# Optimization experiments

Hardware: AMD Instinct MI355X
Metric: run time of the kernel (lower is better)

Reference implementation:

```python
import jax, jax.numpy as jnp
import numpy as np

N_NODES = 50000
N_EDGES = 800000
IN_FEATS = 128
H_FEATS = 128
NUM_CLASSES = 16


def setup_inputs() -> dict:
    key = jax.random.key(0)
    ks = jax.random.split(key, 10)
    in_feat = jax.random.normal(ks[0], (N_NODES, IN_FEATS), dtype=jnp.float32)
    src = jax.random.randint(ks[1], (N_EDGES,), 0, N_NODES, dtype=jnp.int64)
    dst = jax.random.randint(ks[2], (N_EDGES,), 0, N_NODES, dtype=jnp.int64)
    def glorot(k, shape):
        lim = np.sqrt(6.0 / (shape[0] + shape[1]))
        return jax.random.uniform(k, shape, jnp.float32, -lim, lim)
    W_self1 = glorot(ks[3], (IN_FEATS, H_FEATS))
    W_neigh1 = glorot(ks[4], (IN_FEATS, H_FEATS))
    b1 = jnp.zeros((H_FEATS,), jnp.float32)
    W_self2 = glorot(ks[5], (H_FEATS, NUM_CLASSES))
    W_neigh2 = glorot(ks[6], (H_FEATS, NUM_CLASSES))
    b2 = jnp.zeros((NUM_CLASSES,), jnp.float32)
    return {"in_feat": in_feat, "src": src, "dst": dst,
            "W_self1": W_self1, "W_neigh1": W_neigh1, "b1": b1,
            "W_self2": W_self2, "W_neigh2": W_neigh2, "b2": b2}


def _mean_agg(h, src, dst, n_nodes):
    # sum of source features at each destination node, divided by in-degree
    summed = jax.ops.segment_sum(h[src], dst, num_segments=n_nodes)  # [N, d]
    deg = jax.ops.segment_sum(jnp.ones_like(dst, dtype=h.dtype), dst,
                              num_segments=n_nodes)                   # [N]
    return summed / jnp.maximum(deg, 1.0)[:, None]


def _sage_conv(h, src, dst, W_self, W_neigh, b):
    h_neigh = _mean_agg(h, src, dst, h.shape[0])
    return h @ W_self + h_neigh @ W_neigh + b


def reference(in_feat, src, dst, W_self1, W_neigh1, b1, W_self2, W_neigh2, b2):
    h = _sage_conv(in_feat, src, dst, W_self1, W_neigh1, b1)
    h = jax.nn.relu(h)
    h = _sage_conv(h, src, dst, W_self2, W_neigh2, b2)
    return h
```

## Files before the change

kernel.cpp:

```cpp
#include <hip/hip_runtime.h>

#define NF 128
#define BSH 8
#define CHUNK 4096

typedef __attribute__((ext_vector_type(8))) short short8;
typedef __attribute__((ext_vector_type(4))) float floatx4;

__device__ __forceinline__ unsigned short f2bf(float f) {
    unsigned u = __float_as_uint(f);
    u += 0x7fff + ((u >> 16) & 1);
    return (unsigned short)(u >> 16);
}
__device__ __forceinline__ unsigned pk2(float a, float b) {
    return (unsigned)f2bf(a) | ((unsigned)f2bf(b) << 16);
}
__device__ __forceinline__ float bflo(unsigned u) { return __uint_as_float(u << 16); }
__device__ __forceinline__ float bfhi(unsigned u) { return __uint_as_float(u & 0xffff0000u); }

__device__ __forceinline__ unsigned enc8(float f) {
    unsigned b = __float_as_uint(f);
    unsigned s = (b >> 24) & 0x80u;
    b &= 0x7fffffffu;
    unsigned t = b + 0x7FFFFu + ((b >> 20) & 1u);
    unsigned m = (t >= 0x3C800000u) ? (((t - 0x3C000000u) >> 20) & 0x7Fu) : 0u;
    return s | m;
}
__device__ __forceinline__ void dec4(float* acc, unsigned w) {
#pragma unroll
    for (int j = 0; j < 4; ++j) {
        unsigned u = (w >> (8 * j)) & 0xffu;
        acc[j] += __uint_as_float(((u & 0x80u) << 24) | ((u & 0x7fu) << 20));
    }
}


__global__ __launch_bounds__(256) void k_prep(const float* __restrict__ in_feat,
                                              const int* __restrict__ dst,
                                              const float* __restrict__ Ws1,
                                              const float* __restrict__ Wn1,
                                              const float* __restrict__ Ws2,
                                              const float* __restrict__ Wn2,
                                              unsigned short* __restrict__ featbf,
                                              unsigned char* __restrict__ feat8,
                                              unsigned short* __restrict__ W1t,
                                              unsigned short* __restrict__ W2t,
                                              int* __restrict__ cnt2,
                                              int nb_cvt, int nb_w, int E) {
    int b = blockIdx.x, tid = threadIdx.x;
    if (b < nb_cvt) {
        int i = b * 256 + tid;
        const float4* p = (const float4*)in_feat + (size_t)i * 2;
        float4 a = p[0], c = p[1];
        uint4 o;
        o.x = pk2(a.x, a.y); o.y = pk2(a.z, a.w);
        o.z = pk2(c.x, c.y); o.w = pk2(c.z, c.w);
        ((uint4*)featbf)[i] = o;
        uint2 q;
        q.x = enc8(a.x) | (enc8(a.y) << 8) | (enc8(a.z) << 16) | (enc8(a.w) << 24);
        q.y = enc8(c.x) | (enc8(c.y) << 8) | (enc8(c.z) << 16) | (enc8(c.w) << 24);
        ((uint2*)feat8)[i] = q;
    } else if (b < nb_cvt + nb_w) {
        int idx = (b - nb_cvt) * 256 + tid;
        if (idx < 128 * 256) {
            int n = idx >> 8, kk = idx & 255;
            float v = (kk < 128) ? Ws1[(size_t)kk * 128 + n]
                                 : Wn1[(size_t)(kk - 128) * 128 + n];
            W1t[idx] = f2bf(v);
        } else {
            int idx2 = idx - 128 * 256;
            if (idx2 < 32 * 128) {
                int n = idx2 >> 7, k = idx2 & 127;
                float v = (n < 16) ? Ws2[(size_t)k * 16 + n]
                                   : Wn2[(size_t)k * 16 + (n - 16)];
                W2t[idx2] = f2bf(v);
            }
        }
    } else {
        __shared__ int h[256];
        int c = b - nb_cvt - nb_w;
        h[tid] = 0;
        __syncthreads();
        int base = c * CHUNK;
        int n = min(CHUNK, E - base);
        for (int i = tid; i < n; i += 256) atomicAdd(&h[dst[base + i] >> BSH], 1);
        __syncthreads();
        cnt2[c * 256 + tid] = h[tid];
    }
}


__global__ __launch_bounds__(256) void k_cscan(const int* __restrict__ cnt2,
                                               int* __restrict__ goff,
                                               int* __restrict__ basep, int nc) {
    __shared__ int sw[4];
    int tid = threadIdx.x, lane = tid & 63, w = tid >> 6;
    int tot = 0;
    int c = 0;
    for (; c + 7 < nc; c += 8) {
        int v0 = cnt2[(c + 0) * 256 + tid], v1 = cnt2[(c + 1) * 256 + tid];
        int v2 = cnt2[(c + 2) * 256 + tid], v3 = cnt2[(c + 3) * 256 + tid];
        int v4 = cnt2[(c + 4) * 256 + tid], v5 = cnt2[(c + 5) * 256 + tid];
        int v6 = cnt2[(c + 6) * 256 + tid], v7 = cnt2[(c + 7) * 256 + tid];
        tot += ((v0 + v1) + (v2 + v3)) + ((v4 + v5) + (v6 + v7));
    }
    for (; c < nc; ++c) tot += cnt2[c * 256 + tid];

    int inc = tot;
#pragma unroll
    for (int d = 1; d < 64; d <<= 1) {
        int t = __shfl_up(inc, (unsigned)d, 64);
        if (lane >= d) inc += t;
    }
    if (lane == 63) sw[w] = inc;
    __syncthreads();
    int add = 0;
    for (int i = 0; i < w; ++i) add += sw[i];
    int ex = add + inc - tot;
    goff[tid] = ex;
    if (tid == 255) goff[256] = ex + tot;

    int run = ex;
    for (c = 0; c < nc; c += 8) {
        int v[8];
#pragma unroll
        for (int j = 0; j < 8; ++j)
            v[j] = (c + j < nc) ? cnt2[(c + j) * 256 + tid] : 0;
#pragma unroll
        for (int j = 0; j < 8; ++j) {
            if (c + j < nc) basep[(c + j) * 256 + tid] = run;
            run += v[j];
        }
    }
}


__global__ __launch_bounds__(256) void k_part(const int* __restrict__ src,
                                              const int* __restrict__ dst,
                                              const int* __restrict__ basep,
                                              unsigned* __restrict__ ebuf, int E) {
    __shared__ int cur[256];
    int tid = threadIdx.x;
    cur[tid] = basep[blockIdx.x * 256 + tid];
    __syncthreads();
    int base = blockIdx.x * CHUNK;
    int n = min(CHUNK, E - base);
    for (int i = tid; i < n; i += 256) {
        int dd = dst[base + i];
        int p = atomicAdd(&cur[dd >> BSH], 1);
        ebuf[p] = ((unsigned)(dd & 255) << 16) | (unsigned)src[base + i];
    }
}


__global__ __launch_bounds__(256) void k_fine(const unsigned* __restrict__ ebuf,
                                              const int* __restrict__ goff,
                                              int* __restrict__ off,
                                              int* __restrict__ csr, int N) {
    __shared__ int degL[256];
    __shared__ int offL[256];
    __shared__ int sw[4];
    int b = blockIdx.x, tid = threadIdx.x;
    int node0 = b << BSH;
    int e0 = goff[b], e1 = goff[b + 1];
    degL[tid] = 0;
    __syncthreads();
    for (int e = e0 + tid; e < e1; e += 256) atomicAdd(&degL[ebuf[e] >> 16], 1);
    __syncthreads();
    int lane = tid & 63, w = tid >> 6;
    int v = degL[tid], inc = v;
#pragma unroll
    for (int d = 1; d < 64; d <<= 1) {
        int t = __shfl_up(inc, (unsigned)d, 64);
        if (lane >= d) inc += t;
    }
    if (lane == 63) sw[w] = inc;
    __syncthreads();
    int add = 0;
    for (int i = 0; i < w; ++i) add += sw[i];
    int ex = add + inc - v;
    offL[tid] = ex;
    int idx = node0 + tid;
    if (idx <= N) off[idx] = e0 + ex;
    degL[tid] = 0;
    __syncthreads();
    for (int e = e0 + tid; e < e1; e += 256) {
        unsigned u = ebuf[e];
        int d = u >> 16;
        int pos = e0 + offL[d] + atomicAdd(&degL[d], 1);
        csr[pos] = (int)(u & 0xffffu);
    }
}


__global__ __launch_bounds__(256, 6) void k_agg1(const unsigned char* __restrict__ feat8,
                                                 const int* __restrict__ off,
                                                 const int* __restrict__ csr,
                                                 unsigned short* __restrict__ hn1,
                                                 int N, int pb) {
    int b = blockIdx.x;
    int half = (b >= pb) ? 1 : 0;
    int idx = (b - half * pb) * 256 + threadIdx.x;
    int g = idx >> 3;
    int lane = idx & 7;
    if (g >= N) return;
    int s0 = off[g], s1 = off[g + 1];
    const unsigned char* base = feat8 + half * 64 + lane * 8;
    float acc[8];
#pragma unroll
    for (int i = 0; i < 8; ++i) acc[i] = 0.f;
    int e = s0;
    for (; e + 7 < s1; e += 8) {
        uint2 v0 = *(const uint2*)(base + (size_t)csr[e + 0] * 128);
        uint2 v1 = *(const uint2*)(base + (size_t)csr[e + 1] * 128);
        uint2 v2 = *(const uint2*)(base + (size_t)csr[e + 2] * 128);
        uint2 v3 = *(const uint2*)(base + (size_t)csr[e + 3] * 128);
        uint2 v4 = *(const uint2*)(base + (size_t)csr[e + 4] * 128);
        uint2 v5 = *(const uint2*)(base + (size_t)csr[e + 5] * 128);
        uint2 v6 = *(const uint2*)(base + (size_t)csr[e + 6] * 128);
        uint2 v7 = *(const uint2*)(base + (size_t)csr[e + 7] * 128);
        dec4(acc + 0, v0.x); dec4(acc + 4, v0.y);
        dec4(acc + 0, v1.x); dec4(acc + 4, v1.y);
        dec4(acc + 0, v2.x); dec4(acc + 4, v2.y);
        dec4(acc + 0, v3.x); dec4(acc + 4, v3.y);
        dec4(acc + 0, v4.x); dec4(acc + 4, v4.y);
        dec4(acc + 0, v5.x); dec4(acc + 4, v5.y);
        dec4(acc + 0, v6.x); dec4(acc + 4, v6.y);
        dec4(acc + 0, v7.x); dec4(acc + 4, v7.y);
    }
    if (e + 3 < s1) {
        uint2 v0 = *(const uint2*)(base + (size_t)csr[e + 0] * 128);
        uint2 v1 = *(const uint2*)(base + (size_t)csr[e + 1] * 128);
        uint2 v2 = *(const uint2*)(base + (size_t)csr[e + 2] * 128);
        uint2 v3 = *(const uint2*)(base + (size_t)csr[e + 3] * 128);
        dec4(acc + 0, v0.x); dec4(acc + 4, v0.y);
        dec4(acc + 0, v1.x); dec4(acc + 4, v1.y);
        dec4(acc + 0, v2.x); dec4(acc + 4, v2.y);
        dec4(acc + 0, v3.x); dec4(acc + 4, v3.y);
        e += 4;
    }
    for (; e < s1; ++e) {
        uint2 v = *(const uint2*)(base + (size_t)csr[e] * 128);
        dec4(acc + 0, v.x); dec4(acc + 4, v.y);
    }
    float inv = __uint_as_float(0x7B800000u) / fmaxf((float)(s1 - s0), 1.0f);
    uint4 o;
    o.x = pk2(acc[0] * inv, acc[1] * inv);
    o.y = pk2(acc[2] * inv, acc[3] * inv);
    o.z = pk2(acc[4] * inv, acc[5] * inv);
    o.w = pk2(acc[6] * inv, acc[7] * inv);
    *(uint4*)(hn1 + (size_t)g * NF + half * 64 + lane * 8) = o;
}


__global__ __launch_bounds__(256) void k_gemm(const unsigned short* __restrict__ Abf,
                                              const unsigned short* __restrict__ Hbf,
                                              const unsigned short* __restrict__ W1t,
                                              const float* __restrict__ b1,
                                              const unsigned short* __restrict__ W2t,
                                              const float* __restrict__ b2,
                                              float* __restrict__ t2s,
                                              unsigned short* __restrict__ t2n, int M) {
    __shared__ float hL[64 * 140];
    int tid = threadIdx.x;
    int w = tid >> 6, lane = tid & 63;
    int q = lane >> 4, r = lane & 15;
    int row = blockIdx.x * 64 + w * 16 + r;
    int rowc = min(row, M - 1);

    floatx4 acc[8];
#pragma unroll
    for (int t = 0; t < 8; ++t) acc[t] = (floatx4){0.f, 0.f, 0.f, 0.f};

    const unsigned short* arow = Abf + (size_t)rowc * 128;
    const unsigned short* hrow = Hbf + (size_t)rowc * 128;

#pragma unroll
    for (int kc = 0; kc < 8; ++kc) {
        const unsigned short* ap = (kc < 4) ? (arow + kc * 32 + q * 8)
                                            : (hrow + (kc - 4) * 32 + q * 8);
        short8 a = *(const short8*)ap;
        const unsigned short* wp = W1t + kc * 32 + q * 8 + (size_t)r * 256;
#pragma unroll
        for (int t = 0; t < 8; ++t) {
            short8 b = *(const short8*)(wp + (size_t)t * 16 * 256);
            acc[t] = __builtin_amdgcn_mfma_f32_16x16x32_bf16(a, b, acc[t], 0, 0, 0);
        }
    }

#pragma unroll
    for (int i = 0; i < 4; ++i) {
        int lr = w * 16 + q * 4 + i;
#pragma unroll
        for (int t = 0; t < 8; ++t)
            hL[lr * 140 + t * 16 + r] = fmaxf(acc[t][i] + b1[t * 16 + r], 0.0f);
    }

    floatx4 acc2[2];
#pragma unroll
    for (int t = 0; t < 2; ++t) acc2[t] = (floatx4){0.f, 0.f, 0.f, 0.f};

#pragma unroll
    for (int kc = 0; kc < 4; ++kc) {
        const float* pa = hL + (w * 16 + r) * 140 + kc * 32 + q * 8;
        float4 fa = *(const float4*)pa;
        float4 fb = *(const float4*)(pa + 4);
        union { short8 s; uint4 u; } cv;
        cv.u = make_uint4(pk2(fa.x, fa.y), pk2(fa.z, fa.w),
                          pk2(fb.x, fb.y), pk2(fb.z, fb.w));
        const unsigned short* wp = W2t + kc * 32 + q * 8 + (size_t)r * 128;
#pragma unroll
        for (int t = 0; t < 2; ++t) {
            short8 b = *(const short8*)(wp + (size_t)t * 16 * 128);
            acc2[t] = __builtin_amdgcn_mfma_f32_16x16x32_bf16(cv.s, b, acc2[t], 0, 0, 0);
        }
    }

    int orow0 = blockIdx.x * 64 + w * 16 + q * 4;
    float bb = b2[r];
#pragma unroll
    for (int i = 0; i < 4; ++i) {
        int orow = orow0 + i;
        if (orow < M) {
            t2s[(size_t)orow * 16 + r] = acc2[0][i] + bb;
            t2n[(size_t)orow * 16 + r] = f2bf(acc2[1][i]);
        }
    }
}


__global__ __launch_bounds__(256, 8) void k_out(const float* __restrict__ t2s,
                                                const unsigned short* __restrict__ t2n,
                                                const int* __restrict__ off,
                                                const int* __restrict__ csr,
                                                float* __restrict__ out, int N) {
    int idx = blockIdx.x * 256 + threadIdx.x;
    int node = idx >> 2;
    if (node >= N) return;
    int ln = idx & 3;
    int s0 = off[node], s1 = off[node + 1];
    float acc[4];
#pragma unroll
    for (int i = 0; i < 4; ++i) acc[i] = 0.f;
    const uint2* T = (const uint2*)t2n;
    int e = s0;
    for (; e + 7 < s1; e += 8) {
        uint2 v0 = T[(size_t)csr[e + 0] * 4 + ln];
        uint2 v1 = T[(size_t)csr[e + 1] * 4 + ln];
        uint2 v2 = T[(size_t)csr[e + 2] * 4 + ln];
        uint2 v3 = T[(size_t)csr[e + 3] * 4 + ln];
        uint2 v4 = T[(size_t)csr[e + 4] * 4 + ln];
        uint2 v5 = T[(size_t)csr[e + 5] * 4 + ln];
        uint2 v6 = T[(size_t)csr[e + 6] * 4 + ln];
        uint2 v7 = T[(size_t)csr[e + 7] * 4 + ln];
        acc[0] += bflo(v0.x) + bflo(v1.x) + bflo(v2.x) + bflo(v3.x)
                + bflo(v4.x) + bflo(v5.x) + bflo(v6.x) + bflo(v7.x);
        acc[1] += bfhi(v0.x) + bfhi(v1.x) + bfhi(v2.x) + bfhi(v3.x)
                + bfhi(v4.x) + bfhi(v5.x) + bfhi(v6.x) + bfhi(v7.x);
        acc[2] += bflo(v0.y) + bflo(v1.y) + bflo(v2.y) + bflo(v3.y)
                + bflo(v4.y) + bflo(v5.y) + bflo(v6.y) + bflo(v7.y);
        acc[3] += bfhi(v0.y) + bfhi(v1.y) + bfhi(v2.y) + bfhi(v3.y)
                + bfhi(v4.y) + bfhi(v5.y) + bfhi(v6.y) + bfhi(v7.y);
    }
    for (; e < s1; ++e) {
        uint2 v = T[(size_t)csr[e] * 4 + ln];
        acc[0] += bflo(v.x); acc[1] += bfhi(v.x);
        acc[2] += bflo(v.y); acc[3] += bfhi(v.y);
    }
    float inv = 1.0f / fmaxf((float)(s1 - s0), 1.0f);
    const float4* sp = (const float4*)(t2s + (size_t)node * 16 + ln * 4);
    float4 sv = sp[0];
    float4 r;
    r.x = sv.x + acc[0] * inv;
    r.y = sv.y + acc[1] * inv;
    r.z = sv.z + acc[2] * inv;
    r.w = sv.w + acc[3] * inv;
    *(float4*)(out + (size_t)node * 16 + ln * 4) = r;
}


extern "C" void kernel_launch(void* const* d_in, const int* in_sizes, int n_in,
                              void* d_out, int out_size, void* d_ws, size_t ws_size,
                              hipStream_t stream) {
    const float* in_feat = (const float*)d_in[0];
    const int*   src     = (const int*)d_in[1];
    const int*   dst     = (const int*)d_in[2];
    const float* Ws1     = (const float*)d_in[3];
    const float* Wn1     = (const float*)d_in[4];
    const float* b1      = (const float*)d_in[5];
    const float* Ws2     = (const float*)d_in[6];
    const float* Wn2     = (const float*)d_in[7];
    const float* b2      = (const float*)d_in[8];
    float* outp = (float*)d_out;

    int N = in_sizes[0] / NF;
    int E = in_sizes[1];
    int nb = (N + 255) >> BSH;
    int nc = (E + CHUNK - 1) / CHUNK;

    char* ws = (char*)d_ws;
    size_t o = 0;
    auto alloc = [&](size_t bytes) -> char* {
        char* p = ws + o;
        o = (o + bytes + 255) & ~(size_t)255;
        return p;
    };
    int*      cnt2  = (int*)alloc((size_t)nc * 256 * 4);
    int*      basep = (int*)alloc((size_t)nc * 256 * 4);
    int*      goff  = (int*)alloc(257 * 4);
    int*      off   = (int*)alloc((size_t)(N + 1) * 4);
    int*      csr   = (int*)alloc((size_t)E * 4);
    unsigned* ebuf  = (unsigned*)alloc((size_t)E * 4);
    unsigned short* featbf = (unsigned short*)alloc((size_t)N * NF * 2);
    unsigned char*  feat8  = (unsigned char*)alloc((size_t)N * NF);
    unsigned short* hn1    = (unsigned short*)alloc((size_t)N * NF * 2);
    unsigned short* W1t    = (unsigned short*)alloc((size_t)128 * 256 * 2);
    unsigned short* W2t    = (unsigned short*)alloc((size_t)32 * 128 * 2);
    float*          t2s    = (float*)alloc((size_t)N * 16 * 4);
    unsigned short* t2n    = (unsigned short*)alloc((size_t)N * 16 * 2);

    int nb_cvt = (N * NF / 8 + 255) / 256;
    int nb_w = (128 * 256 + 32 * 128 + 255) / 256;
    k_prep<<<nb_cvt + nb_w + nc, 256, 0, stream>>>(in_feat, dst, Ws1, Wn1, Ws2, Wn2,
                                                   featbf, feat8, W1t, W2t, cnt2,
                                                   nb_cvt, nb_w, E);
    k_cscan<<<1, 256, 0, stream>>>(cnt2, goff, basep, nc);
    k_part<<<nc, 256, 0, stream>>>(src, dst, basep, ebuf, E);
    k_fine<<<nb, 256, 0, stream>>>(ebuf, goff, off, csr, N);

    int pb = (N * 8 + 255) / 256;
    k_agg1<<<pb * 2, 256, 0, stream>>>(feat8, off, csr, hn1, N, pb);

    int gb_m = (N + 63) / 64;
    k_gemm<<<gb_m, 256, 0, stream>>>(featbf, hn1, W1t, b1, W2t, b2, t2s, t2n, N);
    k_out<<<(N * 4 + 255) / 256, 256, 0, stream>>>(t2s, t2n, off, csr, outp, N);
}
```

Measured before the change: 222.0 us.

## Compress CSR indices to 16-bit and gather full 128B rows per aggregation thread

Stores CSR source indices as unsigned short instead of int, halving the index traffic read by both aggregation kernels. This relies on N fitting in 16 bits, which the edge buffer encoding already assumes. The first-layer aggregation no longer splits each row into two half-passes. Each 8-lane group now loads the whole 128-byte fp8 row with 16-byte loads into 16 accumulators, so the index list is read once instead of twice, at the cost of more registers per thread. The partition chunk size is also halved to raise parallelism in the partitioning kernel.

```diff
diff --git a/kernel.cpp b/kernel.cpp
--- a/kernel.cpp
+++ b/kernel.cpp
@@ -2,7 +2,7 @@
 
 #define NF 128
 #define BSH 8
-#define CHUNK 4096
+#define CHUNK 2048
 
 typedef __attribute__((ext_vector_type(8))) short short8;
 typedef __attribute__((ext_vector_type(4))) float floatx4;
@@ -156,7 +156,7 @@
 __global__ __launch_bounds__(256) void k_fine(const unsigned* __restrict__ ebuf,
                                               const int* __restrict__ goff,
                                               int* __restrict__ off,
-                                              int* __restrict__ csr, int N) {
+                                              unsigned short* __restrict__ csr, int N) {
     __shared__ int degL[256];
     __shared__ int offL[256];
     __shared__ int sw[4];
@@ -188,68 +188,52 @@
         unsigned u = ebuf[e];
         int d = u >> 16;
         int pos = e0 + offL[d] + atomicAdd(&degL[d], 1);
-        csr[pos] = (int)(u & 0xffffu);
-    }
-}
-
-
-__global__ __launch_bounds__(256, 6) void k_agg1(const unsigned char* __restrict__ feat8,
+        csr[pos] = (unsigned short)(u & 0xffffu);
+    }
+}
+
+
+__global__ __launch_bounds__(256, 8) void k_agg1(const unsigned char* __restrict__ feat8,
                                                  const int* __restrict__ off,
-                                                 const int* __restrict__ csr,
-                                                 unsigned short* __restrict__ hn1,
-                                                 int N, int pb) {
-    int b = blockIdx.x;
-    int half = (b >= pb) ? 1 : 0;
-    int idx = (b - half * pb) * 256 + threadIdx.x;
+                                                 const unsigned short* __restrict__ csr,
+                                                 unsigned short* __restrict__ hn1, int N) {
+    int idx = blockIdx.x * 256 + threadIdx.x;
     int g = idx >> 3;
     int lane = idx & 7;
     if (g >= N) return;
     int s0 = off[g], s1 = off[g + 1];
-    const unsigned char* base = feat8 + half * 64 + lane * 8;
-    float acc[8];
-#pragma unroll
-    for (int i = 0; i < 8; ++i) acc[i] = 0.f;
+    float acc[16];
+#pragma unroll
+    for (int i = 0; i < 16; ++i) acc[i] = 0.f;
+    const uint4* F = (const uint4*)feat8;
     int e = s0;
-    for (; e + 7 < s1; e += 8) {
-        uint2 v0 = *(const uint2*)(base + (size_t)csr[e + 0] * 128);
-        uint2 v1 = *(const uint2*)(base + (size_t)csr[e + 1] * 128);
-        uint2 v2 = *(const uint2*)(base + (size_t)csr[e + 2] * 128);
-        uint2 v3 = *(const uint2*)(base + (size_t)csr[e + 3] * 128);
-        uint2 v4 = *(const uint2*)(base + (size_t)csr[e + 4] * 128);
-        uint2 v5 = *(const uint2*)(base + (size_t)csr[e + 5] * 128);
-        uint2 v6 = *(const uint2*)(base + (size_t)csr[e + 6] * 128);
-        uint2 v7 = *(const uint2*)(base + (size_t)csr[e + 7] * 128);
-        dec4(acc + 0, v0.x); dec4(acc + 4, v0.y);
-        dec4(acc + 0, v1.x); dec4(acc + 4, v1.y);
-        dec4(acc + 0, v2.x); dec4(acc + 4, v2.y);
-        dec4(acc + 0, v3.x); dec4(acc + 4, v3.y);
-        dec4(acc + 0, v4.x); dec4(acc + 4, v4.y);
-        dec4(acc + 0, v5.x); dec4(acc + 4, v5.y);
-        dec4(acc + 0, v6.x); dec4(acc + 4, v6.y);
-        dec4(acc + 0, v7.x); dec4(acc + 4, v7.y);
-    }
-    if (e + 3 < s1) {
-        uint2 v0 = *(const uint2*)(base + (size_t)csr[e + 0] * 128);
-        uint2 v1 = *(const uint2*)(base + (size_t)csr[e + 1] * 128);
-        uint2 v2 = *(const uint2*)(base + (size_t)csr[e + 2] * 128);
-        uint2 v3 = *(const uint2*)(base + (size_t)csr[e + 3] * 128);
-        dec4(acc + 0, v0.x); dec4(acc + 4, v0.y);
-        dec4(acc + 0, v1.x); dec4(acc + 4, v1.y);
-        dec4(acc + 0, v2.x); dec4(acc + 4, v2.y);
-        dec4(acc + 0, v3.x); dec4(acc + 4, v3.y);
-        e += 4;
+    for (; e + 3 < s1; e += 4) {
+        uint4 v0 = F[(size_t)csr[e + 0] * 8 + lane];
+        uint4 v1 = F[(size_t)csr[e + 1] * 8 + lane];
+        uint4 v2 = F[(size_t)csr[e + 2] * 8 + lane];
+        uint4 v3 = F[(size_t)csr[e + 3] * 8 + lane];
+        dec4(acc + 0, v0.x); dec4(acc + 4, v0.y); dec4(acc + 8, v0.z); dec4(acc + 12, v0.w);
+        dec4(acc + 0, v1.x); dec4(acc + 4, v1.y); dec4(acc + 8, v1.z); dec4(acc + 12, v1.w);
+        dec4(acc + 0, v2.x); dec4(acc + 4, v2.y); dec4(acc + 8, v2.z); dec4(acc + 12, v2.w);
+        dec4(acc + 0, v3.x); dec4(acc + 4, v3.y); dec4(acc + 8, v3.z); dec4(acc + 12, v3.w);
     }
     for (; e < s1; ++e) {
-        uint2 v = *(const uint2*)(base + (size_t)csr[e] * 128);
-        dec4(acc + 0, v.x); dec4(acc + 4, v.y);
+        uint4 v = F[(size_t)csr[e] * 8 + lane];
+        dec4(acc + 0, v.x); dec4(acc + 4, v.y); dec4(acc + 8, v.z); dec4(acc + 12, v.w);
     }
     float inv = __uint_as_float(0x7B800000u) / fmaxf((float)(s1 - s0), 1.0f);
-    uint4 o;
-    o.x = pk2(acc[0] * inv, acc[1] * inv);
-    o.y = pk2(acc[2] * inv, acc[3] * inv);
-    o.z = pk2(acc[4] * inv, acc[5] * inv);
-    o.w = pk2(acc[6] * inv, acc[7] * inv);
-    *(uint4*)(hn1 + (size_t)g * NF + half * 64 + lane * 8) = o;
+    uint4 o0, o1;
+    o0.x = pk2(acc[0] * inv, acc[1] * inv);
+    o0.y = pk2(acc[2] * inv, acc[3] * inv);
+    o0.z = pk2(acc[4] * inv, acc[5] * inv);
+    o0.w = pk2(acc[6] * inv, acc[7] * inv);
+    o1.x = pk2(acc[8] * inv, acc[9] * inv);
+    o1.y = pk2(acc[10] * inv, acc[11] * inv);
+    o1.z = pk2(acc[12] * inv, acc[13] * inv);
+    o1.w = pk2(acc[14] * inv, acc[15] * inv);
+    uint4* op = (uint4*)(hn1 + (size_t)g * NF + lane * 16);
+    op[0] = o0;
+    op[1] = o1;
 }
 
 
@@ -332,7 +316,7 @@
 __global__ __launch_bounds__(256, 8) void k_out(const float* __restrict__ t2s,
                                                 const unsigned short* __restrict__ t2n,
                                                 const int* __restrict__ off,
-                                                const int* __restrict__ csr,
+                                                const unsigned short* __restrict__ csr,
                                                 float* __restrict__ out, int N) {
     int idx = blockIdx.x * 256 + threadIdx.x;
     int node = idx >> 2;
@@ -409,7 +393,7 @@
     int*      basep = (int*)alloc((size_t)nc * 256 * 4);
     int*      goff  = (int*)alloc(257 * 4);
     int*      off   = (int*)alloc((size_t)(N + 1) * 4);
-    int*      csr   = (int*)alloc((size_t)E * 4);
+    unsigned short* csr = (unsigned short*)alloc((size_t)E * 2);
     unsigned* ebuf  = (unsigned*)alloc((size_t)E * 4);
     unsigned short* featbf = (unsigned short*)alloc((size_t)N * NF * 2);
     unsigned char*  feat8  = (unsigned char*)alloc((size_t)N * NF);
@@ -428,8 +412,7 @@
     k_part<<<nc, 256, 0, stream>>>(src, dst, basep, ebuf, E);
     k_fine<<<nb, 256, 0, stream>>>(ebuf, goff, off, csr, N);
 
-    int pb = (N * 8 + 255) / 256;
-    k_agg1<<<pb * 2, 256, 0, stream>>>(feat8, off, csr, hn1, N, pb);
+    k_agg1<<<(N * 8 + 255) / 256, 256, 0, stream>>>(feat8, off, csr, hn1, N);
 
     int gb_m = (N + 63) / 64;
     k_gemm<<<gb_m, 256, 0, stream>>>(featbf, hn1, W1t, b1, W2t, b2, t2s, t2n, N);
```

Result: slower. 244.1 us (+9.9%).
